# Performance work log

Measured on AMD Instinct MI355X. Metric: run time of the kernel, lower is better.

The kernel has to match this reference:

```python
import jax, jax.numpy as jnp
import numpy as np

EPS = 1e-5  # torch BatchNorm2d default eps

# BinaryActivation with STE: grad zeroed where |x| >= 1 (the extra 1.3 clip in
# xnor_binarize.backward is a subset and thus redundant).
@jax.custom_vjp
def sign_act(x):
    return jnp.sign(x)

def _sa_fwd(x):
    return jnp.sign(x), x

def _sa_bwd(x, g):
    mask = ((x > -1.0) & (x < 1.0)).astype(g.dtype)
    return (g * mask,)

sign_act.defvjp(_sa_fwd, _sa_bwd)

# Weight binarization (scale=False path): w.data.clamp_(-1,1) then sign();
# backward is straight-through identity (|bi_weight|=1 < 1.3 so clip never fires).
@jax.custom_vjp
def bin_weight(w):
    return jnp.sign(jnp.clip(w, -1.0, 1.0))

def _bw_fwd(w):
    return jnp.sign(jnp.clip(w, -1.0, 1.0)), None

def _bw_bwd(_, g):
    return (g,)

bin_weight.defvjp(_bw_fwd, _bw_bwd)


def _branch(x, gamma, beta, w, bias):
    # BatchNorm2d (training-mode batch stats, biased var), affine
    mu = jnp.mean(x, axis=(0, 2, 3), keepdims=True)
    var = jnp.var(x, axis=(0, 2, 3), keepdims=True)
    h = (x - mu) * jax.lax.rsqrt(var + EPS)
    h = h * gamma[None, :, None, None] + beta[None, :, None, None]
    # XNOR conv: binarized activations and weights, stride 2, pad 1
    a = sign_act(h)
    bw = bin_weight(w)
    y = jax.lax.conv_general_dilated(
        a, bw, window_strides=(2, 2), padding=[(1, 1), (1, 1)],
        dimension_numbers=('NCHW', 'OIHW', 'NCHW'))
    y = y + bias[None, :, None, None]
    # shortcut: AvgPool2d(kernel_size=2) (stride defaults to 2)
    B, C, H, W = x.shape
    sc = x.reshape(B, C, H // 2, 2, W // 2, 2).mean(axis=(3, 5))
    return jax.nn.relu(y) + sc


def setup_inputs() -> dict:
    key = jax.random.key(0)
    ks = jax.random.split(key, 9)
    B, C, H, W = 32, 192, 64, 64
    K = 3
    x = jax.random.normal(ks[0], (B, C, H, W), dtype=jnp.float32)
    g1 = 1.0 + 0.1 * jax.random.normal(ks[1], (C,), dtype=jnp.float32)
    b1 = 0.1 * jax.random.normal(ks[2], (C,), dtype=jnp.float32)
    w1 = 0.05 * jax.random.normal(ks[3], (C, C, K, K), dtype=jnp.float32)
    bias1 = jnp.zeros((C,), dtype=jnp.float32)
    g2 = 1.0 + 0.1 * jax.random.normal(ks[4], (C,), dtype=jnp.float32)
    b2 = 0.1 * jax.random.normal(ks[5], (C,), dtype=jnp.float32)
    w2 = 0.05 * jax.random.normal(ks[6], (C, C, K, K), dtype=jnp.float32)
    bias2 = jnp.zeros((C,), dtype=jnp.float32)
    return {"x": x, "g1": g1, "b1": b1, "w1": w1, "bias1": bias1,
            "g2": g2, "b2": b2, "w2": w2, "bias2": bias2}


def reference(x, g1, b1, w1, bias1, g2, b2, w2, bias2):
    x1 = _branch(x, g1, b1, w1, bias1)
    x2 = _branch(x, g2, b2, w2, bias2)
    return jnp.concatenate([x1, x2], axis=1)  # [B, 2C, H/2, W/2]
```

## Files before the change

### kernel.cpp

```cpp
#include <hip/hip_runtime.h>

typedef unsigned int u32;

#define BN 32
#define CC 192
#define HH 64
#define WW 64
#define HWSZ (HH*WW)
#define OHH 32
#define OWW 32
#define NVALID_SCALE 131072.0f
#define PLH 65
#define PLW2 66
#define PLSZ (PLH*PLW2)
#define NPLANE (12*BN)
#define NSTATS (CC*BN)
#define NPW (2*CC)
#define WROW 56

__global__ __launch_bounds__(256) void k_front(const float* __restrict__ x,
        float* __restrict__ partial,
        const float* __restrict__ w1, const float* __restrict__ w2,
        u32* __restrict__ wp, u32* __restrict__ wsum,
        u32* __restrict__ act) {
    __shared__ float red[8];
    __shared__ float wl[CC * 9];
    __shared__ u32 ww[54];
    int blk = blockIdx.x;
    int tid = threadIdx.x;
    if (blk < NSTATS) {
        int c = blk >> 5, n = blk & 31;
        const float4* p = (const float4*)(x + ((size_t)(n * CC + c) << 12));
        float s = 0.f, s2 = 0.f;
#pragma unroll
        for (int k = 0; k < 4; ++k) {
            float4 f = p[tid + 256 * k];
            s  += f.x + f.y + f.z + f.w;
            s2 += f.x * f.x + f.y * f.y + f.z * f.z + f.w * f.w;
        }
#pragma unroll
        for (int off = 32; off > 0; off >>= 1) {
            s  += __shfl_down(s, off, 64);
            s2 += __shfl_down(s2, off, 64);
        }
        int wv = tid >> 6, ln = tid & 63;
        if (ln == 0) { red[wv * 2] = s; red[wv * 2 + 1] = s2; }
        __syncthreads();
        if (tid == 0) {
            partial[blk * 2]     = red[0] + red[2] + red[4] + red[6];
            partial[blk * 2 + 1] = red[1] + red[3] + red[5] + red[7];
        }
    } else if (blk < NSTATS + NPW) {
        int b  = blk - NSTATS;
        int br = b / CC, oc = b - br * CC;
        const float* W = (br ? w2 : w1) + (size_t)oc * CC * 9;
        for (int i = tid; i < CC * 9; i += 256) wl[i] = W[i];
        __syncthreads();
        if (tid < WROW) {
            u32 word = 0;
            if (tid < 54) {
                int w6 = tid % 6, pos = tid / 6;
#pragma unroll
                for (int bb = 0; bb < 32; ++bb) {
                    if (wl[(w6 * 32 + bb) * 9 + pos] > 0.f) word |= (1u << bb);
                }
                ww[tid] = word;
            }
            wp[(size_t)b * WROW + tid] = word;
        }
        __syncthreads();
        if (tid == 0) {
            int Wt[9];
#pragma unroll
            for (int t = 0; t < 9; ++t) {
                int s = 0;
#pragma unroll
                for (int w6 = 0; w6 < 6; ++w6) s += __popc(ww[t * 6 + w6]);
                Wt[t] = s;
            }
            wsum[b * 4 + 0] = (u32)(Wt[0] + Wt[1] + Wt[2]);
            wsum[b * 4 + 1] = (u32)(Wt[0] + Wt[3] + Wt[6]);
            wsum[b * 4 + 2] = (u32)Wt[0];
            wsum[b * 4 + 3] = 0;
        }
    } else {
        int plane = blk - NSTATS - NPW;
        u32* pl = act + (size_t)plane * PLSZ;
        if (tid < PLW2) pl[tid] = 0;
        else if (tid < PLW2 + 64) pl[(tid - PLW2 + 1) * PLW2 + 1] = 0;
    }
}

__global__ __launch_bounds__(64) void k_coef(const float* __restrict__ partial,
        const float* __restrict__ g1, const float* __restrict__ b1,
        const float* __restrict__ g2, const float* __restrict__ b2,
        float* __restrict__ coef) {
    int c = blockIdx.x;
    int t = threadIdx.x;
    int half = t >> 5, i = t & 31;
    float v = partial[(c * 32 + i) * 2 + half];
#pragma unroll
    for (int off = 16; off > 0; off >>= 1) v += __shfl_down(v, off, 32);
    float S2 = __shfl(v, 32, 64);
    if (t == 0) {
        float S = v;
        const float inv = 1.0f / NVALID_SCALE;
        float mu  = S * inv;
        float var = S2 * inv - mu * mu;
        float r   = 1.0f / sqrtf(var + 1e-5f);
        float s1 = g1[c] * r, t1 = b1[c] - mu * s1;
        float s2 = g2[c] * r, t2 = b2[c] - mu * s2;
        ((float4*)coef)[c] = make_float4(s1, t1, s2, t2);
    }
}

__global__ __launch_bounds__(256) void k_pack_act(const float* __restrict__ x,
        const float* __restrict__ coef, u32* __restrict__ act,
        float* __restrict__ scb) {
    int bx = blockIdx.x;
    int g  = blockIdx.y;
    int n = bx >> 2, q = bx & 3;
    int tid = threadIdx.x;
    int ow = tid & 31, oh = (q << 3) + (tid >> 5);
    const float4* c4 = (const float4*)coef;
    const float* xb = x + (size_t)n * CC * HWSZ + (size_t)(2 * oh) * WW + 2 * ow;
    float* scp = scb + ((size_t)(n * CC + g * 32) * OHH + oh) * OWW + ow;
    u32 pk[8] = {0, 0, 0, 0, 0, 0, 0, 0};
#pragma unroll 4
    for (int bb = 0; bb < 32; ++bb) {
        int ch = g * 32 + bb;
        const float* p = xb + (size_t)ch * HWSZ;
        float2 r0 = *(const float2*)p;
        float2 r1 = *(const float2*)(p + WW);
        scp[(size_t)bb * (OHH * OWW)] = (r0.x + r0.y + r1.x + r1.y) * 0.25f;
        float4 cf = c4[ch];
        u32 bit = 1u << bb;
        if (r0.x * cf.x + cf.y > 0.f) pk[0] |= bit;
        if (r0.y * cf.x + cf.y > 0.f) pk[1] |= bit;
        if (r1.x * cf.x + cf.y > 0.f) pk[2] |= bit;
        if (r1.y * cf.x + cf.y > 0.f) pk[3] |= bit;
        if (r0.x * cf.z + cf.w > 0.f) pk[4] |= bit;
        if (r0.y * cf.z + cf.w > 0.f) pk[5] |= bit;
        if (r1.x * cf.z + cf.w > 0.f) pk[6] |= bit;
        if (r1.y * cf.z + cf.w > 0.f) pk[7] |= bit;
    }
    size_t o00 = (size_t)(2 * oh + 1) * PLW2 + (2 * ow + 2);
    u32* a1 = act + ((size_t)(0 * 6 + g) * BN + n) * PLSZ + o00;
    u32* a2 = act + ((size_t)(1 * 6 + g) * BN + n) * PLSZ + o00;
    *(uint2*)a1            = make_uint2(pk[0], pk[1]);
    *(uint2*)(a1 + PLW2)   = make_uint2(pk[2], pk[3]);
    *(uint2*)a2            = make_uint2(pk[4], pk[5]);
    *(uint2*)(a2 + PLW2)   = make_uint2(pk[6], pk[7]);
}

__global__ __launch_bounds__(256) void k_conv(
        const u32* __restrict__ act, const u32* __restrict__ wp,
        const uint4* __restrict__ wsum4, const float* __restrict__ scb,
        const float* __restrict__ bias1, const float* __restrict__ bias2,
        float* __restrict__ out) {
    int b    = blockIdx.x;
    int tile = b >> 2;
    int n    = tile >> 4, ohp = tile & 15;
    int wid  = __builtin_amdgcn_readfirstlane((int)(threadIdx.x >> 6));
    int ocbase = ((b & 3) * 4 + wid) * 12;
    int lane = threadIdx.x & 63;
    int ow = lane & 31, lh = lane >> 5;
    int oh = 2 * ohp + lh;
    int lbase = (2 * oh) * PLW2 + 2 * ow + 1;
    int topE  = (oh == 0), leftE = (ow == 0);
    int nv192 = CC * ((topE ? 2 : 3) * (leftE ? 2 : 3));
    float sc[12];
#pragma unroll 1
    for (int br = 0; br < 2; ++br) {
        u32 a[WROW];
        const u32* ap = act + ((size_t)(br * 6) * BN + n) * PLSZ + lbase;
#pragma unroll
        for (int w6 = 0; w6 < 6; ++w6) {
            const u32* app = ap + (size_t)w6 * (BN * PLSZ);
#pragma unroll
            for (int t = 0; t < 9; ++t) {
                a[t * 6 + w6] = app[(t / 3) * PLW2 + (t % 3)];
            }
        }
        a[54] = 0u; a[55] = 0u;
        const uint4*  wq4 = (const uint4*)(wp + (size_t)(br * CC + ocbase) * WROW);
        const uint4*  ws4 = wsum4 + (br * CC + ocbase);
        const float*  bsp = (br ? bias2 : bias1) + ocbase;
#pragma unroll 1
        for (int j = 0; j < 12; ++j) {
            const uint4* wr = wq4 + j * (WROW / 4);
            int p = 0;
#pragma unroll
            for (int k = 0; k < WROW / 4; ++k) {
                uint4 w4 = wr[k];
                p += __popc(a[4 * k + 0] ^ w4.x);
                p += __popc(a[4 * k + 1] ^ w4.y);
                p += __popc(a[4 * k + 2] ^ w4.z);
                p += __popc(a[4 * k + 3] ^ w4.w);
            }
            uint4 wsv = ws4[j];
            int corr = (topE ? (int)wsv.x : 0) + (leftE ? (int)wsv.y : 0)
                     - ((topE & leftE) ? (int)wsv.z : 0);
            int dot = nv192 - 2 * p + 2 * corr;
            int oc = ocbase + j;
            float y = (float)dot + bsp[j];
            if (br == 0) {
                sc[j] = scb[((size_t)(n * CC + oc) * OHH + oh) * OWW + ow];
            }
            __builtin_nontemporal_store(fmaxf(y, 0.f) + sc[j],
                &out[((size_t)(n * 384 + br * CC + oc) * OHH + oh) * OWW + ow]);
        }
    }
}

extern "C" void kernel_launch(void* const* d_in, const int* in_sizes, int n_in,
                              void* d_out, int out_size, void* d_ws, size_t ws_size,
                              hipStream_t stream) {
    const float* x     = (const float*)d_in[0];
    const float* g1    = (const float*)d_in[1];
    const float* b1    = (const float*)d_in[2];
    const float* w1    = (const float*)d_in[3];
    const float* bias1 = (const float*)d_in[4];
    const float* g2    = (const float*)d_in[5];
    const float* b2    = (const float*)d_in[6];
    const float* w2    = (const float*)d_in[7];
    const float* bias2 = (const float*)d_in[8];
    float* out = (float*)d_out;
    char* ws = (char*)d_ws;
    float* partial = (float*)(ws);
    float* coef    = (float*)(ws + 49152);
    u32*   wp      = (u32*)  (ws + 52224);
    u32*   wsum    = (u32*)  (ws + 138240);
    float* scb     = (float*)(ws + 144384);
    u32*   act     = (u32*)  (ws + 25310208);

    hipLaunchKernelGGL(k_front,   dim3(NSTATS + NPW + NPLANE), dim3(256), 0, stream,
                       x, partial, w1, w2, wp, wsum, act);
    hipLaunchKernelGGL(k_coef,    dim3(CC),          dim3(64),  0, stream,
                       partial, g1, b1, g2, b2, coef);
    hipLaunchKernelGGL(k_pack_act, dim3(128, 6),     dim3(256), 0, stream,
                       x, coef, act, scb);
    hipLaunchKernelGGL(k_conv,    dim3(BN * 16 * 4), dim3(256), 0, stream,
                       act, wp, (const uint4*)wsum, scb, bias1, bias2, out);
}
```

Before: 251.7 us.

## Restructure binary conv loop to keep 12 accumulators and stream activations per word group

The packed weight layout changes to [branch][word-group][oc][12], and the conv loop order is inverted. Each thread now loads 9 activation words per 32-channel group and accumulates popcounts for all 12 output channels at once, instead of holding 56 activation words in registers and looping over output channels. The goal is lower register pressure and better occupancy, with weight loads becoming scalar-friendly per group. In exchange the shortcut values are reloaded for each branch rather than cached, the weight reads are no longer uint4 vector loads, and the workspace offsets are shifted to fit the larger weight buffer.

```diff
diff --git a/kernel.cpp b/kernel.cpp
--- a/kernel.cpp
+++ b/kernel.cpp
@@ -16,7 +16,7 @@
 #define NPLANE (12*BN)
 #define NSTATS (CC*BN)
 #define NPW (2*CC)
-#define WROW 56
+#define WSTR 12
 
 __global__ __launch_bounds__(256) void k_front(const float* __restrict__ x,
         float* __restrict__ partial,
@@ -56,17 +56,17 @@
         const float* W = (br ? w2 : w1) + (size_t)oc * CC * 9;
         for (int i = tid; i < CC * 9; i += 256) wl[i] = W[i];
         __syncthreads();
-        if (tid < WROW) {
+        if (tid < 72) {
+            int w6 = tid / 12, pos = tid % 12;
             u32 word = 0;
-            if (tid < 54) {
-                int w6 = tid % 6, pos = tid / 6;
+            if (pos < 9) {
 #pragma unroll
                 for (int bb = 0; bb < 32; ++bb) {
                     if (wl[(w6 * 32 + bb) * 9 + pos] > 0.f) word |= (1u << bb);
                 }
-                ww[tid] = word;
+                ww[w6 * 9 + pos] = word;
             }
-            wp[(size_t)b * WROW + tid] = word;
+            wp[((size_t)(br * 6 + w6) * CC + oc) * WSTR + pos] = word;
         }
         __syncthreads();
         if (tid == 0) {
@@ -75,7 +75,7 @@
             for (int t = 0; t < 9; ++t) {
                 int s = 0;
 #pragma unroll
-                for (int w6 = 0; w6 < 6; ++w6) s += __popc(ww[t * 6 + w6]);
+                for (int w6 = 0; w6 < 6; ++w6) s += __popc(ww[w6 * 9 + t]);
                 Wt[t] = s;
             }
             wsum[b * 4 + 0] = (u32)(Wt[0] + Wt[1] + Wt[2]);
@@ -169,45 +169,40 @@
     int lbase = (2 * oh) * PLW2 + 2 * ow + 1;
     int topE  = (oh == 0), leftE = (ow == 0);
     int nv192 = CC * ((topE ? 2 : 3) * (leftE ? 2 : 3));
-    float sc[12];
 #pragma unroll 1
     for (int br = 0; br < 2; ++br) {
-        u32 a[WROW];
-        const u32* ap = act + ((size_t)(br * 6) * BN + n) * PLSZ + lbase;
-#pragma unroll
+        int p[12];
+#pragma unroll
+        for (int j = 0; j < 12; ++j) p[j] = 0;
+        const u32* ap  = act + ((size_t)(br * 6) * BN + n) * PLSZ + lbase;
+        const u32* wqb = wp + ((size_t)(br * 6) * CC + ocbase) * WSTR;
+#pragma unroll 2
         for (int w6 = 0; w6 < 6; ++w6) {
             const u32* app = ap + (size_t)w6 * (BN * PLSZ);
-#pragma unroll
-            for (int t = 0; t < 9; ++t) {
-                a[t * 6 + w6] = app[(t / 3) * PLW2 + (t % 3)];
+            u32 a[9];
+#pragma unroll
+            for (int t = 0; t < 9; ++t) a[t] = app[(t / 3) * PLW2 + (t % 3)];
+            const u32* wr = wqb + (size_t)w6 * (CC * WSTR);
+#pragma unroll
+            for (int j = 0; j < 12; ++j) {
+#pragma unroll
+                for (int t = 0; t < 9; ++t) {
+                    p[j] += __popc(a[t] ^ wr[j * WSTR + t]);
+                }
             }
         }
-        a[54] = 0u; a[55] = 0u;
-        const uint4*  wq4 = (const uint4*)(wp + (size_t)(br * CC + ocbase) * WROW);
         const uint4*  ws4 = wsum4 + (br * CC + ocbase);
         const float*  bsp = (br ? bias2 : bias1) + ocbase;
-#pragma unroll 1
+#pragma unroll
         for (int j = 0; j < 12; ++j) {
-            const uint4* wr = wq4 + j * (WROW / 4);
-            int p = 0;
-#pragma unroll
-            for (int k = 0; k < WROW / 4; ++k) {
-                uint4 w4 = wr[k];
-                p += __popc(a[4 * k + 0] ^ w4.x);
-                p += __popc(a[4 * k + 1] ^ w4.y);
-                p += __popc(a[4 * k + 2] ^ w4.z);
-                p += __popc(a[4 * k + 3] ^ w4.w);
-            }
             uint4 wsv = ws4[j];
             int corr = (topE ? (int)wsv.x : 0) + (leftE ? (int)wsv.y : 0)
                      - ((topE & leftE) ? (int)wsv.z : 0);
-            int dot = nv192 - 2 * p + 2 * corr;
+            int dot = nv192 - 2 * p[j] + 2 * corr;
             int oc = ocbase + j;
             float y = (float)dot + bsp[j];
-            if (br == 0) {
-                sc[j] = scb[((size_t)(n * CC + oc) * OHH + oh) * OWW + ow];
-            }
-            __builtin_nontemporal_store(fmaxf(y, 0.f) + sc[j],
+            float sc = scb[((size_t)(n * CC + oc) * OHH + oh) * OWW + ow];
+            __builtin_nontemporal_store(fmaxf(y, 0.f) + sc,
                 &out[((size_t)(n * 384 + br * CC + oc) * OHH + oh) * OWW + ow]);
         }
     }
@@ -230,9 +225,9 @@
     float* partial = (float*)(ws);
     float* coef    = (float*)(ws + 49152);
     u32*   wp      = (u32*)  (ws + 52224);
-    u32*   wsum    = (u32*)  (ws + 138240);
-    float* scb     = (float*)(ws + 144384);
-    u32*   act     = (u32*)  (ws + 25310208);
+    u32*   wsum    = (u32*)  (ws + 162816);
+    float* scb     = (float*)(ws + 168960);
+    u32*   act     = (u32*)  (ws + 25334784);
 
     hipLaunchKernelGGL(k_front,   dim3(NSTATS + NPW + NPLANE), dim3(256), 0, stream,
                        x, partial, w1, w2, wp, wsum, act);
```

Result: faster. 242.8 us (-3.5%).
